# Performance work log

Measured on AMD Instinct MI355X. Metric: run time of the kernel, lower is better.

## Reference

```python
import jax, jax.numpy as jnp
import numpy as np

N_NODES = 100000
N_EDGES = 1200000
N_GRAPHS = 1024
IN_FEATS = 64
HID = 64
BN_EPS = 1e-5


def setup_inputs() -> dict:
    key = jax.random.key(0)
    ks = jax.random.split(key, 20)
    feats = jax.random.normal(ks[0], (N_NODES, IN_FEATS), jnp.float32)
    src = jax.random.randint(ks[1], (N_EDGES,), 0, N_NODES, jnp.int32)
    dst = jax.random.randint(ks[2], (N_EDGES,), 0, N_NODES, jnp.int32)
    graph_ids = jnp.sort(jax.random.randint(ks[3], (N_NODES,), 0, N_GRAPHS, jnp.int32))

    def lin(k, fi, fo):
        s = 1.0 / np.sqrt(fi)
        kw, kb = jax.random.split(k)
        return (jax.random.uniform(kw, (fi, fo), jnp.float32, -s, s),
                jax.random.uniform(kb, (fo,), jnp.float32, -s, s))

    W_self, _ = lin(ks[4], IN_FEATS, HID)
    W_neigh, b_neigh = lin(ks[5], IN_FEATS, HID)
    W1, b1 = lin(ks[6], HID, 128)
    W2, b2 = lin(ks[7], 128, 64)
    W3, b3 = lin(ks[8], 64, 1)

    def bn(k, d):
        k1, k2, k3, k4 = jax.random.split(k, 4)
        return (jax.random.normal(k1, (d,), jnp.float32) * 0.1 + 1.0,
                jax.random.normal(k2, (d,), jnp.float32) * 0.1,
                jax.random.normal(k3, (d,), jnp.float32) * 0.1,
                jax.random.uniform(k4, (d,), jnp.float32, 0.5, 1.5))

    g1, be1, rm1, rv1 = bn(ks[9], 128)
    g2, be2, rm2, rv2 = bn(ks[10], 64)

    return dict(feats=feats, src=src, dst=dst, graph_ids=graph_ids,
                W_self=W_self, W_neigh=W_neigh, b_neigh=b_neigh,
                W1=W1, b1=b1, g1=g1, be1=be1, rm1=rm1, rv1=rv1,
                W2=W2, b2=b2, g2=g2, be2=be2, rm2=rm2, rv2=rv2,
                W3=W3, b3=b3)


def reference(feats, src, dst, graph_ids, W_self, W_neigh, b_neigh,
              W1, b1, g1, be1, rm1, rv1, W2, b2, g2, be2, rm2, rv2, W3, b3):
    # --- SAGEConv (mean aggregator): h = W_self@h_self + W_neigh@mean_neigh + b
    deg = jax.ops.segment_sum(jnp.ones((src.shape[0],), feats.dtype), dst,
                              num_segments=N_NODES)                      # [N]
    agg = jax.ops.segment_sum(feats[src], dst, num_segments=N_NODES)     # [N, F]
    mean_neigh = agg / jnp.maximum(deg, 1.0)[:, None]
    h = feats @ W_self + mean_neigh @ W_neigh + b_neigh
    h = jax.nn.relu(h)                                                   # activation

    # --- per-graph max readout (dgl.max_nodes)
    hg = jax.ops.segment_max(h, graph_ids, num_segments=N_GRAPHS)        # [G, HID]

    # --- MLP head with eval-mode BatchNorm1d
    def bn(x, g, b, rm, rv):
        return (x - rm) * jax.lax.rsqrt(rv + BN_EPS) * g + b

    x = bn(jax.nn.relu(hg @ W1 + b1), g1, be1, rm1, rv1)
    x = bn(jax.nn.relu(x @ W2 + b2), g2, be2, rm2, rv2)
    return x @ W3 + b3                                                   # [G, n_task]
```

## Files before the change

### kernel.cpp

```cpp
#include <hip/hip_runtime.h>
#include <hip/hip_fp16.h>

#define N_NODES  100000
#define N_EDGES  1200000
#define N_GRAPHS 1024
#define F        64
#define BN_EPS   1e-5f
#define NBUCK    ((N_NODES + 255) / 256)
#define NBLK     512
#define CHUNK    ((N_EDGES + NBLK - 1) / NBLK)
#define MT       128
#define GEMM_BLOCKS ((N_NODES + MT - 1) / MT)
#define CE       3584
#define LDA      72

typedef _Float16 f16x8 __attribute__((ext_vector_type(8)));
typedef float f32x4 __attribute__((ext_vector_type(4)));

__global__ __launch_bounds__(256) void prepscat(
    const float* __restrict__ feats, const float* __restrict__ Wself,
    const float* __restrict__ Wneigh, __half* __restrict__ Uh,
    __half* __restrict__ Zh, const int* __restrict__ src,
    const int* __restrict__ dst, int* __restrict__ gcur,
    int* __restrict__ pairs) {
  __shared__ __align__(16) char smraw[2 * 128 * LDA * 2];
  int t = threadIdx.x;

  if (blockIdx.x < NBLK) {
    int* dcache = (int*)smraw;
    int* lh   = dcache + CHUNK;
    int* lcur = lh + NBUCK;
    int b = blockIdx.x;
    for (int i = t; i < NBUCK; i += 256) lh[i] = 0;
    __syncthreads();
    int e0 = b * CHUNK, e1 = e0 + CHUNK;
    if (e1 > N_EDGES) e1 = N_EDGES;
    for (int e = e0 + t; e < e1; e += 256) {
      int d = dst[e];
      dcache[e - e0] = d;
      atomicAdd(&lh[d >> 8], 1);
    }
    __syncthreads();
    for (int i = t; i < NBUCK; i += 256) {
      int c = lh[i];
      lcur[i] = c ? atomicAdd(&gcur[i], c) : 0;
    }
    __syncthreads();
    for (int e = e0 + t; e < e1; e += 256) {
      int d = dcache[e - e0];
      int pos = atomicAdd(&lcur[d >> 8], 1);
      if (pos < CE)
        pairs[(size_t)(d >> 8) * CE + pos] =
            (int)((((unsigned)d & 255u) << 24) | (unsigned)src[e]);
    }
    return;
  }

  __half* As = (__half*)smraw;
  __half* Bs = As + 128 * LDA;
  int mbase = (blockIdx.x - NBLK) * MT;

#pragma unroll
  for (int s = 0; s < 8; s++) {
    int idx = s * 256 + t;
    int row = idx >> 4, c4 = idx & 15;
    int gm = mbase + row;
    float4 v = (gm < N_NODES) ? *(const float4*)(feats + (size_t)gm * F + c4 * 4)
                              : make_float4(0.f, 0.f, 0.f, 0.f);
    union { __half h[4]; uint2 u; } pk;
    pk.h[0] = __float2half_rn(v.x); pk.h[1] = __float2half_rn(v.y);
    pk.h[2] = __float2half_rn(v.z); pk.h[3] = __float2half_rn(v.w);
    *(uint2*)(As + row * LDA + c4 * 4) = pk.u;
  }

#pragma unroll
  for (int s = 0; s < 2; s++) {
    int unit = s * 256 + t;
    int kq = unit >> 5, c4 = unit & 31;
    const float* Wp = (c4 < 16) ? (Wself + c4 * 4) : (Wneigh + (c4 - 16) * 4);
    float4 w0 = *(const float4*)(Wp + (kq * 4 + 0) * 64);
    float4 w1 = *(const float4*)(Wp + (kq * 4 + 1) * 64);
    float4 w2 = *(const float4*)(Wp + (kq * 4 + 2) * 64);
    float4 w3 = *(const float4*)(Wp + (kq * 4 + 3) * 64);
    float a[4][4] = {{w0.x, w0.y, w0.z, w0.w}, {w1.x, w1.y, w1.z, w1.w},
                     {w2.x, w2.y, w2.z, w2.w}, {w3.x, w3.y, w3.z, w3.w}};
#pragma unroll
    for (int c = 0; c < 4; c++) {
      union { __half h[4]; uint2 u; } pk;
      pk.h[0] = __float2half_rn(a[0][c]); pk.h[1] = __float2half_rn(a[1][c]);
      pk.h[2] = __float2half_rn(a[2][c]); pk.h[3] = __float2half_rn(a[3][c]);
      *(uint2*)(Bs + (c4 * 4 + c) * LDA + kq * 4) = pk.u;
    }
  }
  __syncthreads();

  int wave = t >> 6, lane = t & 63;
  int lr = lane & 15, kg = lane >> 4;
  int r0 = wave * 32;

  f32x4 acc[2][8];
#pragma unroll
  for (int i = 0; i < 2; i++)
#pragma unroll
    for (int j = 0; j < 8; j++) acc[i][j] = (f32x4){0.f, 0.f, 0.f, 0.f};

#pragma unroll
  for (int h = 0; h < 2; h++) {
    f16x8 a0 = *(const f16x8*)(As + (r0 + lr) * LDA + h * 32 + kg * 8);
    f16x8 a1 = *(const f16x8*)(As + (r0 + 16 + lr) * LDA + h * 32 + kg * 8);
#pragma unroll
    for (int j = 0; j < 8; j++) {
      f16x8 wv = *(const f16x8*)(Bs + (j * 16 + lr) * LDA + h * 32 + kg * 8);
      acc[0][j] = __builtin_amdgcn_mfma_f32_16x16x32_f16(wv, a0, acc[0][j], 0, 0, 0);
      acc[1][j] = __builtin_amdgcn_mfma_f32_16x16x32_f16(wv, a1, acc[1][j], 0, 0, 0);
    }
  }

#pragma unroll
  for (int i = 0; i < 2; i++) {
    int node = mbase + r0 + i * 16 + lr;
    if (node < N_NODES) {
#pragma unroll
      for (int j = 0; j < 8; j++) {
        int f = j * 16 + kg * 4;
        union { __half h[4]; uint2 u; } pk;
        pk.h[0] = __float2half_rn(acc[i][j][0]);
        pk.h[1] = __float2half_rn(acc[i][j][1]);
        pk.h[2] = __float2half_rn(acc[i][j][2]);
        pk.h[3] = __float2half_rn(acc[i][j][3]);
        __half* outp = (f < 64) ? (Uh + (size_t)node * F + f)
                                : (Zh + (size_t)node * F + (f - 64));
        *(uint2*)outp = pk.u;
      }
    }
  }
}

__global__ __launch_bounds__(1024) void gather_place(
    const __half* __restrict__ Uh, const __half* __restrict__ Zh,
    const int* __restrict__ pairs, const int* __restrict__ gcur,
    const float* __restrict__ bneigh, const int* __restrict__ gids,
    int* __restrict__ hgbits) {
  __shared__ int eidx_l[CE];
  __shared__ int rsl[256];
  __shared__ int lh[256];
  __shared__ int cur[256];
  int b = blockIdx.x, t = threadIdx.x;
  int nb0 = b << 8;
  const int* pr = pairs + (size_t)b * CE;
  int E = gcur[b]; if (E > CE) E = CE;

  if (t < 256) lh[t] = 0;
  __syncthreads();
  for (int e = t; e < E; e += 1024)
    atomicAdd(&lh[((unsigned)pr[e]) >> 24], 1);
  __syncthreads();
  if (t < 256) cur[t] = lh[t];
  __syncthreads();
  for (int off = 1; off < 256; off <<= 1) {
    int u = (t < 256 && t >= off) ? cur[t - off] : 0;
    __syncthreads();
    if (t < 256) cur[t] += u;
    __syncthreads();
  }
  if (t < 256) { int ex = cur[t] - lh[t]; rsl[t] = ex; cur[t] = ex; }
  __syncthreads();
  for (int e = t; e < E; e += 1024) {
    unsigned p = (unsigned)pr[e];
    int pos = atomicAdd(&cur[p >> 24], 1);
    eidx_l[pos] = (int)(p & 0xFFFFFFu);
  }
  __syncthreads();

  int wave = t >> 6, lane = t & 63;
  int fl = lane & 15, sub = lane >> 4;
  float4 b4 = *(const float4*)(bneigh + 4 * fl);
  int nl = wave * 16;
  int nend = nl + 16;
  if (nb0 + nl >= N_NODES) return;
  if (nb0 + nend > N_NODES) nend = N_NODES - nb0;

  int curg = gids[nb0 + nl];
  float4 gmax = {0.f, 0.f, 0.f, 0.f};

  for (; nl < nend; nl++) {
    int node = nb0 + nl;
    int rr  = rsl[nl];
    int deg = lh[nl];
    uint2 ur = *(const uint2*)(Uh + (size_t)node * F + 4 * fl);
    float sx = 0.f, sy = 0.f, sz = 0.f, sw = 0.f;
    for (int jj = 0; jj < deg; jj += 16) {
      int j0 = jj + sub;
      int s0 = (j0      < deg) ? eidx_l[rr + j0]      : 0;
      int s1 = (j0 + 4  < deg) ? eidx_l[rr + j0 + 4]  : 0;
      int s2 = (j0 + 8  < deg) ? eidx_l[rr + j0 + 8]  : 0;
      int s3 = (j0 + 12 < deg) ? eidx_l[rr + j0 + 12] : 0;
      uint2 z0 = *(const uint2*)(Zh + (size_t)s0 * F + 4 * fl);
      uint2 z1 = *(const uint2*)(Zh + (size_t)s1 * F + 4 * fl);
      uint2 z2 = *(const uint2*)(Zh + (size_t)s2 * F + 4 * fl);
      uint2 z3 = *(const uint2*)(Zh + (size_t)s3 * F + 4 * fl);
      if (j0 < deg) {
        float2 f0 = __half22float2(*(__half2*)&z0.x);
        float2 f1 = __half22float2(*(__half2*)&z0.y);
        sx += f0.x; sy += f0.y; sz += f1.x; sw += f1.y;
      }
      if (j0 + 4 < deg) {
        float2 f0 = __half22float2(*(__half2*)&z1.x);
        float2 f1 = __half22float2(*(__half2*)&z1.y);
        sx += f0.x; sy += f0.y; sz += f1.x; sw += f1.y;
      }
      if (j0 + 8 < deg) {
        float2 f0 = __half22float2(*(__half2*)&z2.x);
        float2 f1 = __half22float2(*(__half2*)&z2.y);
        sx += f0.x; sy += f0.y; sz += f1.x; sw += f1.y;
      }
      if (j0 + 12 < deg) {
        float2 f0 = __half22float2(*(__half2*)&z3.x);
        float2 f1 = __half22float2(*(__half2*)&z3.y);
        sx += f0.x; sy += f0.y; sz += f1.x; sw += f1.y;
      }
    }
    sx += __shfl_xor(sx, 16); sy += __shfl_xor(sy, 16);
    sz += __shfl_xor(sz, 16); sw += __shfl_xor(sw, 16);
    sx += __shfl_xor(sx, 32); sy += __shfl_xor(sy, 32);
    sz += __shfl_xor(sz, 32); sw += __shfl_xor(sw, 32);
    float inv = 1.0f / fmaxf((float)deg, 1.0f);

    int g = gids[node];
    if (g != curg) {
      if (sub == 0) {
        int* hp = hgbits + (size_t)curg * F + 4 * fl;
        atomicMax(hp + 0, __float_as_int(gmax.x));
        atomicMax(hp + 1, __float_as_int(gmax.y));
        atomicMax(hp + 2, __float_as_int(gmax.z));
        atomicMax(hp + 3, __float_as_int(gmax.w));
      }
      curg = g; gmax = make_float4(0.f, 0.f, 0.f, 0.f);
    }

    float2 uf0 = __half22float2(*(__half2*)&ur.x);
    float2 uf1 = __half22float2(*(__half2*)&ur.y);
    gmax.x = fmaxf(gmax.x, fmaxf(uf0.x + sx * inv + b4.x, 0.f));
    gmax.y = fmaxf(gmax.y, fmaxf(uf0.y + sy * inv + b4.y, 0.f));
    gmax.z = fmaxf(gmax.z, fmaxf(uf1.x + sz * inv + b4.z, 0.f));
    gmax.w = fmaxf(gmax.w, fmaxf(uf1.y + sw * inv + b4.w, 0.f));
  }
  if (sub == 0) {
    int* hp = hgbits + (size_t)curg * F + 4 * fl;
    atomicMax(hp + 0, __float_as_int(gmax.x));
    atomicMax(hp + 1, __float_as_int(gmax.y));
    atomicMax(hp + 2, __float_as_int(gmax.z));
    atomicMax(hp + 3, __float_as_int(gmax.w));
  }
}

#define GPB 2
__global__ __launch_bounds__(128) void mlp(
    const float* __restrict__ hg,
    const float* __restrict__ W1, const float* __restrict__ b1,
    const float* __restrict__ g1, const float* __restrict__ be1,
    const float* __restrict__ rm1, const float* __restrict__ rv1,
    const float* __restrict__ W2, const float* __restrict__ b2,
    const float* __restrict__ g2, const float* __restrict__ be2,
    const float* __restrict__ rm2, const float* __restrict__ rv2,
    const float* __restrict__ W3, const float* __restrict__ b3,
    float* __restrict__ out) {
  __shared__ float W1s[64 * 128];
  __shared__ float W2s[128 * 64];
  __shared__ float W3s[64];
  __shared__ float sc1[128], sh1[128], b1s[128];
  __shared__ float sc2[64],  sh2[64],  b2s[64];
  __shared__ float s0[64], s1[128], s2[64];
  int t = threadIdx.x;

  for (int i = t; i < 64 * 128; i += 128) W1s[i] = W1[i];
  for (int i = t; i < 128 * 64; i += 128) W2s[i] = W2[i];
  if (t < 64) W3s[t] = W3[t];
  {
    float iv = rsqrtf(rv1[t] + BN_EPS);
    float sc = g1[t] * iv;
    sc1[t] = sc; sh1[t] = be1[t] - rm1[t] * sc; b1s[t] = b1[t];
  }
  if (t < 64) {
    float iv = rsqrtf(rv2[t] + BN_EPS);
    float sc = g2[t] * iv;
    sc2[t] = sc; sh2[t] = be2[t] - rm2[t] * sc; b2s[t] = b2[t];
  }
  __syncthreads();

  for (int gg = 0; gg < GPB; gg++) {
    int g = blockIdx.x * GPB + gg;
    if (t < 64) s0[t] = hg[(size_t)g * F + t];
    __syncthreads();
    {
      float acc = b1s[t];
      for (int i = 0; i < 64; i++) acc += s0[i] * W1s[i * 128 + t];
      acc = fmaxf(acc, 0.0f);
      s1[t] = acc * sc1[t] + sh1[t];
    }
    __syncthreads();
    if (t < 64) {
      float acc = b2s[t];
      for (int i = 0; i < 128; i++) acc += s1[i] * W2s[i * 64 + t];
      acc = fmaxf(acc, 0.0f);
      s2[t] = acc * sc2[t] + sh2[t];
    }
    __syncthreads();
    if (t < 64) {
      float p = s2[t] * W3s[t];
      for (int off = 32; off > 0; off >>= 1) p += __shfl_down(p, off);
      if (t == 0) out[g] = p + b3[0];
    }
    __syncthreads();
  }
}

extern "C" void kernel_launch(void* const* d_in, const int* in_sizes, int n_in,
                              void* d_out, int out_size, void* d_ws, size_t ws_size,
                              hipStream_t stream) {
  const float* feats  = (const float*)d_in[0];
  const int*   src    = (const int*)d_in[1];
  const int*   dst    = (const int*)d_in[2];
  const int*   gids   = (const int*)d_in[3];
  const float* Wself  = (const float*)d_in[4];
  const float* Wneigh = (const float*)d_in[5];
  const float* bneigh = (const float*)d_in[6];
  const float* W1  = (const float*)d_in[7];
  const float* b1  = (const float*)d_in[8];
  const float* g1  = (const float*)d_in[9];
  const float* be1 = (const float*)d_in[10];
  const float* rm1 = (const float*)d_in[11];
  const float* rv1 = (const float*)d_in[12];
  const float* W2  = (const float*)d_in[13];
  const float* b2  = (const float*)d_in[14];
  const float* g2  = (const float*)d_in[15];
  const float* be2 = (const float*)d_in[16];
  const float* rm2 = (const float*)d_in[17];
  const float* rv2 = (const float*)d_in[18];
  const float* W3  = (const float*)d_in[19];
  const float* b3  = (const float*)d_in[20];

  __half* Uh   = (__half*)d_ws;
  __half* Zh   = Uh + (size_t)N_NODES * F;
  int* gcur    = (int*)(Zh + (size_t)N_NODES * F);
  int* hgbits  = gcur + NBUCK;
  int* pairs   = hgbits + (size_t)N_GRAPHS * F;

  hipMemsetAsync(gcur, 0, (NBUCK + N_GRAPHS * F) * sizeof(int), stream);

  prepscat<<<NBLK + GEMM_BLOCKS, 256, 0, stream>>>(feats, Wself, Wneigh,
                                                   Uh, Zh, src, dst, gcur, pairs);
  gather_place<<<NBUCK, 1024, 0, stream>>>(Uh, Zh, pairs, gcur, bneigh,
                                           gids, hgbits);
  mlp<<<N_GRAPHS / GPB, 128, 0, stream>>>((const float*)hgbits,
                                          W1, b1, g1, be1, rm1, rv1,
                                          W2, b2, g2, be2, rm2, rv2, W3, b3,
                                          (float*)d_out);
}
```

Measured before the change: 191.8 us.

## Preconvert weights once and load GEMM operands directly from global memory

Adds a small kernel that converts and transposes the two SAGE weight matrices to fp16 once, so GEMM blocks no longer rebuild them in LDS. GEMM blocks load feature rows straight into registers and read weight fragments from global/L2 with no LDS staging or barrier. GEMM blocks are now scheduled before the edge-scatter blocks, and the scatter uses half as many blocks with larger chunks. The scatter drops its LDS cache of dst and rereads dst from global, trading LDS use for extra global reads and an additional kernel launch.

```diff
diff --git a/kernel.cpp b/kernel.cpp
--- a/kernel.cpp
+++ b/kernel.cpp
@@ -7,39 +7,42 @@
 #define F        64
 #define BN_EPS   1e-5f
 #define NBUCK    ((N_NODES + 255) / 256)
-#define NBLK     512
+#define NBLK     256
 #define CHUNK    ((N_EDGES + NBLK - 1) / NBLK)
 #define MT       128
 #define GEMM_BLOCKS ((N_NODES + MT - 1) / MT)
 #define CE       3584
-#define LDA      72
 
 typedef _Float16 f16x8 __attribute__((ext_vector_type(8)));
 typedef float f32x4 __attribute__((ext_vector_type(4)));
 
+__global__ __launch_bounds__(256) void prepw(
+    const float* __restrict__ Wself, const float* __restrict__ Wneigh,
+    __half* __restrict__ Wh) {
+  int t = threadIdx.x;
+  for (int i = t; i < 128 * 64; i += 256) {
+    int c = i >> 6, k = i & 63;
+    float v = (c < 64) ? Wself[k * 64 + c] : Wneigh[k * 64 + (c - 64)];
+    Wh[i] = __float2half_rn(v);
+  }
+}
+
 __global__ __launch_bounds__(256) void prepscat(
-    const float* __restrict__ feats, const float* __restrict__ Wself,
-    const float* __restrict__ Wneigh, __half* __restrict__ Uh,
-    __half* __restrict__ Zh, const int* __restrict__ src,
-    const int* __restrict__ dst, int* __restrict__ gcur,
-    int* __restrict__ pairs) {
-  __shared__ __align__(16) char smraw[2 * 128 * LDA * 2];
+    const float* __restrict__ feats, const __half* __restrict__ Wh,
+    __half* __restrict__ Uh, __half* __restrict__ Zh,
+    const int* __restrict__ src, const int* __restrict__ dst,
+    int* __restrict__ gcur, int* __restrict__ pairs) {
+  __shared__ int lh[NBUCK];
+  __shared__ int lcur[NBUCK];
   int t = threadIdx.x;
 
-  if (blockIdx.x < NBLK) {
-    int* dcache = (int*)smraw;
-    int* lh   = dcache + CHUNK;
-    int* lcur = lh + NBUCK;
-    int b = blockIdx.x;
+  if (blockIdx.x >= GEMM_BLOCKS) {
+    int b = blockIdx.x - GEMM_BLOCKS;
     for (int i = t; i < NBUCK; i += 256) lh[i] = 0;
     __syncthreads();
     int e0 = b * CHUNK, e1 = e0 + CHUNK;
     if (e1 > N_EDGES) e1 = N_EDGES;
-    for (int e = e0 + t; e < e1; e += 256) {
-      int d = dst[e];
-      dcache[e - e0] = d;
-      atomicAdd(&lh[d >> 8], 1);
-    }
+    for (int e = e0 + t; e < e1; e += 256) atomicAdd(&lh[dst[e] >> 8], 1);
     __syncthreads();
     for (int i = t; i < NBUCK; i += 256) {
       int c = lh[i];
@@ -47,7 +50,7 @@
     }
     __syncthreads();
     for (int e = e0 + t; e < e1; e += 256) {
-      int d = dcache[e - e0];
+      int d = dst[e];
       int pos = atomicAdd(&lcur[d >> 8], 1);
       if (pos < CE)
         pairs[(size_t)(d >> 8) * CE + pos] =
@@ -56,63 +59,45 @@
     return;
   }
 
-  __half* As = (__half*)smraw;
-  __half* Bs = As + 128 * LDA;
-  int mbase = (blockIdx.x - NBLK) * MT;
-
-#pragma unroll
-  for (int s = 0; s < 8; s++) {
-    int idx = s * 256 + t;
-    int row = idx >> 4, c4 = idx & 15;
-    int gm = mbase + row;
-    float4 v = (gm < N_NODES) ? *(const float4*)(feats + (size_t)gm * F + c4 * 4)
-                              : make_float4(0.f, 0.f, 0.f, 0.f);
-    union { __half h[4]; uint2 u; } pk;
-    pk.h[0] = __float2half_rn(v.x); pk.h[1] = __float2half_rn(v.y);
-    pk.h[2] = __float2half_rn(v.z); pk.h[3] = __float2half_rn(v.w);
-    *(uint2*)(As + row * LDA + c4 * 4) = pk.u;
-  }
-
-#pragma unroll
-  for (int s = 0; s < 2; s++) {
-    int unit = s * 256 + t;
-    int kq = unit >> 5, c4 = unit & 31;
-    const float* Wp = (c4 < 16) ? (Wself + c4 * 4) : (Wneigh + (c4 - 16) * 4);
-    float4 w0 = *(const float4*)(Wp + (kq * 4 + 0) * 64);
-    float4 w1 = *(const float4*)(Wp + (kq * 4 + 1) * 64);
-    float4 w2 = *(const float4*)(Wp + (kq * 4 + 2) * 64);
-    float4 w3 = *(const float4*)(Wp + (kq * 4 + 3) * 64);
-    float a[4][4] = {{w0.x, w0.y, w0.z, w0.w}, {w1.x, w1.y, w1.z, w1.w},
-                     {w2.x, w2.y, w2.z, w2.w}, {w3.x, w3.y, w3.z, w3.w}};
-#pragma unroll
-    for (int c = 0; c < 4; c++) {
-      union { __half h[4]; uint2 u; } pk;
-      pk.h[0] = __float2half_rn(a[0][c]); pk.h[1] = __float2half_rn(a[1][c]);
-      pk.h[2] = __float2half_rn(a[2][c]); pk.h[3] = __float2half_rn(a[3][c]);
-      *(uint2*)(Bs + (c4 * 4 + c) * LDA + kq * 4) = pk.u;
-    }
-  }
-  __syncthreads();
-
+  int mbase = blockIdx.x * MT;
   int wave = t >> 6, lane = t & 63;
   int lr = lane & 15, kg = lane >> 4;
   int r0 = wave * 32;
 
+  int n0 = mbase + r0 + lr;
+  int n1 = n0 + 16;
+  int n0c = (n0 < N_NODES) ? n0 : (N_NODES - 1);
+  int n1c = (n1 < N_NODES) ? n1 : (N_NODES - 1);
+  const float* fp0 = feats + (size_t)n0c * F + kg * 8;
+  const float* fp1 = feats + (size_t)n1c * F + kg * 8;
+
+  f16x8 a0[2], a1[2];
+#pragma unroll
+  for (int h = 0; h < 2; h++) {
+    float4 x0 = *(const float4*)(fp0 + h * 32);
+    float4 x1 = *(const float4*)(fp0 + h * 32 + 4);
+    float4 y0 = *(const float4*)(fp1 + h * 32);
+    float4 y1 = *(const float4*)(fp1 + h * 32 + 4);
+    a0[h] = (f16x8){(_Float16)x0.x, (_Float16)x0.y, (_Float16)x0.z, (_Float16)x0.w,
+                    (_Float16)x1.x, (_Float16)x1.y, (_Float16)x1.z, (_Float16)x1.w};
+    a1[h] = (f16x8){(_Float16)y0.x, (_Float16)y0.y, (_Float16)y0.z, (_Float16)y0.w,
+                    (_Float16)y1.x, (_Float16)y1.y, (_Float16)y1.z, (_Float16)y1.w};
+  }
+
   f32x4 acc[2][8];
 #pragma unroll
   for (int i = 0; i < 2; i++)
 #pragma unroll
     for (int j = 0; j < 8; j++) acc[i][j] = (f32x4){0.f, 0.f, 0.f, 0.f};
 
+  const __half* wp = Wh + (size_t)lr * 64 + kg * 8;
 #pragma unroll
   for (int h = 0; h < 2; h++) {
-    f16x8 a0 = *(const f16x8*)(As + (r0 + lr) * LDA + h * 32 + kg * 8);
-    f16x8 a1 = *(const f16x8*)(As + (r0 + 16 + lr) * LDA + h * 32 + kg * 8);
 #pragma unroll
     for (int j = 0; j < 8; j++) {
-      f16x8 wv = *(const f16x8*)(Bs + (j * 16 + lr) * LDA + h * 32 + kg * 8);
-      acc[0][j] = __builtin_amdgcn_mfma_f32_16x16x32_f16(wv, a0, acc[0][j], 0, 0, 0);
-      acc[1][j] = __builtin_amdgcn_mfma_f32_16x16x32_f16(wv, a1, acc[1][j], 0, 0, 0);
+      f16x8 wv = *(const f16x8*)(wp + j * 16 * 64 + h * 32);
+      acc[0][j] = __builtin_amdgcn_mfma_f32_16x16x32_f16(wv, a0[h], acc[0][j], 0, 0, 0);
+      acc[1][j] = __builtin_amdgcn_mfma_f32_16x16x32_f16(wv, a1[h], acc[1][j], 0, 0, 0);
     }
   }
 
@@ -342,14 +327,16 @@
 
   __half* Uh   = (__half*)d_ws;
   __half* Zh   = Uh + (size_t)N_NODES * F;
-  int* gcur    = (int*)(Zh + (size_t)N_NODES * F);
+  __half* Wh   = Zh + (size_t)N_NODES * F;
+  int* gcur    = (int*)(Wh + 128 * 64);
   int* hgbits  = gcur + NBUCK;
   int* pairs   = hgbits + (size_t)N_GRAPHS * F;
 
   hipMemsetAsync(gcur, 0, (NBUCK + N_GRAPHS * F) * sizeof(int), stream);
 
-  prepscat<<<NBLK + GEMM_BLOCKS, 256, 0, stream>>>(feats, Wself, Wneigh,
-                                                   Uh, Zh, src, dst, gcur, pairs);
+  prepw<<<1, 256, 0, stream>>>(Wself, Wneigh, Wh);
+  prepscat<<<GEMM_BLOCKS + NBLK, 256, 0, stream>>>(feats, Wh, Uh, Zh,
+                                                   src, dst, gcur, pairs);
   gather_place<<<NBUCK, 1024, 0, stream>>>(Uh, Zh, pairs, gcur, bneigh,
                                            gids, hgbits);
   mlp<<<N_GRAPHS / GPB, 128, 0, stream>>>((const float*)hgbits,
```

After: 201.2 us. 1.05x slower.
